# Optimization experiments

Measured on AMD Instinct MI355X. Metric: run time of the kernel, lower is better.

Reference implementation:

```python
import jax, jax.numpy as jnp
import numpy as np

N_NODES = 100000
N_EDGES = 1000000
N_GRAPHS = 5000
H = 64
F_IN = 14  # QM9 num_features (11) + pos (3)
BN_EPS = 1e-5


def setup_inputs() -> dict:
    key = jax.random.key(0)
    ks = jax.random.split(key, 16)

    def w(k, shape, fan_in):
        return (jax.random.normal(k, shape, jnp.float32) / np.sqrt(fan_in)).astype(jnp.float32)

    inp = {
        "x": jax.random.normal(ks[0], (N_NODES, 11), jnp.float32),
        "pos": jax.random.normal(ks[1], (N_NODES, 3), jnp.float32),
        "edge_index": jax.random.randint(ks[2], (2, N_EDGES), 0, N_NODES, dtype=jnp.int32),
        "batch": jnp.sort(jax.random.randint(ks[3], (N_NODES,), 0, N_GRAPHS, dtype=jnp.int32)),
    }
    dims = [F_IN, H, H]
    i = 4
    for l, din in enumerate(dims, 1):
        inp[f"w{l}a"] = w(ks[i], (din, H), din); i += 1
        inp[f"b{l}a"] = jnp.zeros((H,), jnp.float32)
        inp[f"g{l}"] = jnp.ones((H,), jnp.float32)   # BatchNorm gamma
        inp[f"be{l}"] = jnp.zeros((H,), jnp.float32)  # BatchNorm beta
        inp[f"w{l}b"] = w(ks[i], (H, H), H); i += 1
        inp[f"b{l}b"] = jnp.zeros((H,), jnp.float32)
    inp["wl1"] = w(ks[i], (3 * H, H), 3 * H); i += 1
    inp["bl1"] = jnp.zeros((H,), jnp.float32)
    inp["wl2"] = w(ks[i], (H, 1), H)
    inp["bl2"] = jnp.zeros((1,), jnp.float32)
    return inp


def _gin_layer(x, src, dst, w1, b1, g, be, w2, b2):
    # GINConv (eps=0): h = MLP(x + sum_{j in N(i)} x_j)
    agg = jax.ops.segment_sum(x[src], dst, num_segments=x.shape[0])
    h = (x + agg) @ w1 + b1
    # BatchNorm1d in training mode: batch stats over node dim (biased var)
    mu = jnp.mean(h, axis=0)
    var = jnp.mean((h - mu) ** 2, axis=0)
    h = jax.nn.relu(g * (h - mu) * jax.lax.rsqrt(var + BN_EPS) + be)
    return jax.nn.relu(h @ w2 + b2)


def _mean_pool(x, batch):
    s = jax.ops.segment_sum(x, batch, num_segments=N_GRAPHS)
    c = jax.ops.segment_sum(jnp.ones((x.shape[0], 1), x.dtype), batch, num_segments=N_GRAPHS)
    return s / jnp.maximum(c, 1.0)


def reference(x, pos, edge_index, batch,
              w1a, b1a, g1, be1, w1b, b1b,
              w2a, b2a, g2, be2, w2b, b2b,
              w3a, b3a, g3, be3, w3b, b3b,
              wl1, bl1, wl2, bl2):
    src, dst = edge_index[0], edge_index[1]
    h0 = jnp.concatenate([x, pos], axis=1)                 # [N, 14]
    x1 = _gin_layer(h0, src, dst, w1a, b1a, g1, be1, w1b, b1b)
    x2 = _gin_layer(x1, src, dst, w2a, b2a, g2, be2, w2b, b2b)
    x3 = _gin_layer(x2, src, dst, w3a, b3a, g3, be3, w3b, b3b)
    p = jnp.concatenate([_mean_pool(x1, batch), _mean_pool(x2, batch), _mean_pool(x3, batch)], axis=1)  # [G, 192]
    h = jax.nn.relu(p @ wl1 + bl1)
    return h @ wl2 + bl2                                   # [G, 1]
```

## Files before the change

### kernel.cpp

```cpp
#include <hip/hip_runtime.h>
#include <hip/hip_bf16.h>

#define BN_EPS 1e-5f
#define LDP 132
#define LDS_BF 72
#define BSH 9
#define EPB 4096

typedef short bf16x8 __attribute__((ext_vector_type(8)));
typedef float f32x4 __attribute__((ext_vector_type(4)));

__device__ __forceinline__ float loadf(const void* p, long long i, unsigned bf) {
    if (bf) return __bfloat162float(((const __hip_bfloat16*)p)[i]);
    return ((const float*)p)[i];
}
__device__ __forceinline__ float b2f(unsigned short u) {
    return __uint_as_float(((unsigned)u) << 16);
}
__device__ __forceinline__ unsigned short f2b(float f) {
    __hip_bfloat16 h = __float2bfloat16(f);
    return *(unsigned short*)&h;
}

__global__ void k_detect(const unsigned* g1w, unsigned* flag) {
    if (threadIdx.x == 0) *flag = (*g1w == 0x3F803F80u) ? 1u : 0u;
}

struct Srcs { const void* p[22]; };

__global__ void k_convert(Srcs s, const unsigned* flag, float* dst) {
    const int sizes[22] = {896,64,64,64,4096,64,  4096,64,64,64,4096,64,
                           4096,64,64,64,4096,64, 12288,64,64,1};
    const int offs[22]  = {0,896,960,1024,1088,5184, 5248,9344,9408,9472,9536,13632,
                           13696,17792,17856,17920,17984,22080, 22144,34432,34496,34560};
    int t = blockIdx.x;
    unsigned bf = *flag;
    const void* src = s.p[t];
    float* d = dst + offs[t];
    int n = sizes[t];
    for (int i = threadIdx.x; i < n; i += blockDim.x) d[i] = loadf(src, i, bf);
}

__global__ __launch_bounds__(256) void k_build(const void* x, const void* pos, const int* batch,
                        const unsigned* flag, float* h0, float* cnt, int N) {
    int i = blockIdx.x * blockDim.x + threadIdx.x;
    if (i >= N) return;
    unsigned bf = *flag;
    float v[14];
    #pragma unroll
    for (int k = 0; k < 11; k++) v[k] = loadf(x, (long long)i * 11 + k, bf);
    #pragma unroll
    for (int k = 0; k < 3; k++) v[11 + k] = loadf(pos, (long long)i * 3 + k, bf);
    #pragma unroll
    for (int k = 0; k < 14; k++) h0[(long long)i*14 + k] = v[k];
    atomicAdd(&cnt[batch[i]], 1.0f);
}

__global__ __launch_bounds__(256) void k_bhist(const int* __restrict__ ei, int* __restrict__ bcnt,
                                               int E, int NCH, int NBK) {
    __shared__ int h[1024];
    int c = blockIdx.x, t = threadIdx.x;
    for (int i = t; i < NBK; i += 256) h[i] = 0;
    __syncthreads();
    int base = c * EPB;
    for (int i = t; i < EPB; i += 256) {
        int e = base + i;
        if (e < E) atomicAdd(&h[ei[E + e] >> BSH], 1);
    }
    __syncthreads();
    for (int i = t; i < NBK; i += 256) bcnt[i * NCH + c] = h[i];
}

__global__ __launch_bounds__(256) void k_scan_partial(const int* __restrict__ src, int* partial, int M) {
    __shared__ int sr[4];
    int b = blockIdx.x, t = threadIdx.x;
    int base = b * 1024;
    int s = 0;
    #pragma unroll
    for (int k = 0; k < 4; k++) {
        int i = base + k * 256 + t;
        if (i < M) s += src[i];
    }
    #pragma unroll
    for (int off = 32; off; off >>= 1) s += __shfl_down(s, off);
    if ((t & 63) == 0) sr[t >> 6] = s;
    __syncthreads();
    if (t == 0) partial[b] = sr[0] + sr[1] + sr[2] + sr[3];
}

__global__ __launch_bounds__(1024) void k_scan_chunks(const int* partial, int* chunkoff, int nchunks) {
    __shared__ int sp[1024];
    int t = threadIdx.x;
    sp[t] = (t < nchunks) ? partial[t] : 0;
    __syncthreads();
    for (int off = 1; off < 1024; off <<= 1) {
        int v = (t >= off) ? sp[t - off] : 0;
        __syncthreads();
        sp[t] += v;
        __syncthreads();
    }
    if (t < nchunks) chunkoff[t] = (t == 0) ? 0 : sp[t - 1];
}

__global__ __launch_bounds__(256) void k_scan_final(const int* __restrict__ src, const int* chunkoff,
                                                    int* __restrict__ out, int M) {
    __shared__ int sp[256];
    int b = blockIdx.x, t = threadIdx.x;
    int base = b * 1024 + t * 4;
    int v0 = 0, v1 = 0, v2 = 0, v3 = 0;
    if (base + 0 < M) v0 = src[base + 0];
    if (base + 1 < M) v1 = src[base + 1];
    if (base + 2 < M) v2 = src[base + 2];
    if (base + 3 < M) v3 = src[base + 3];
    int s = v0 + v1 + v2 + v3;
    sp[t] = s;
    __syncthreads();
    for (int off = 1; off < 256; off <<= 1) {
        int v = (t >= off) ? sp[t - off] : 0;
        __syncthreads();
        sp[t] += v;
        __syncthreads();
    }
    int run = chunkoff[b] + sp[t] - s;
    if (base + 0 < M) { out[base + 0] = run; run += v0; }
    if (base + 1 < M) { out[base + 1] = run; run += v1; }
    if (base + 2 < M) { out[base + 2] = run; run += v2; }
    if (base + 3 < M) { out[base + 3] = run; }
}

__global__ __launch_bounds__(256) void k_place(const int* __restrict__ ei, const int* __restrict__ boff,
                                               int2* __restrict__ ebuf, int E, int NCH, int NBK) {
    __shared__ int cur[1024];
    int c = blockIdx.x, t = threadIdx.x;
    for (int i = t; i < NBK; i += 256) cur[i] = boff[i * NCH + c];
    __syncthreads();
    int base = c * EPB;
    for (int i = t; i < EPB; i += 256) {
        int e = base + i;
        if (e < E) {
            int s = ei[e], d = ei[E + e];
            int pos = atomicAdd(&cur[d >> BSH], 1);
            ebuf[pos] = make_int2(s, d);
        }
    }
}

__global__ __launch_bounds__(256) void k_bucket_fill(const int2* __restrict__ ebuf, const int* __restrict__ boff,
                                                     int* __restrict__ roff, int* __restrict__ csr,
                                                     int N, int E, int NCH, int NBK) {
    __shared__ int cnt[512];
    __shared__ int exc[512];
    __shared__ int curb[512];
    __shared__ int sp[256];
    int b = blockIdx.x, t = threadIdx.x;
    int d0 = b << BSH;
    int dpb = N - d0; if (dpb > 512) dpb = 512;
    int segS = boff[b * NCH];
    int segE = (b + 1 < NBK) ? boff[(b + 1) * NCH] : E;
    cnt[t] = 0; cnt[t + 256] = 0;
    __syncthreads();
    for (int k = segS + t; k < segE; k += 256) atomicAdd(&cnt[ebuf[k].y - d0], 1);
    __syncthreads();
    int a0 = cnt[2 * t], a1 = cnt[2 * t + 1];
    sp[t] = a0 + a1;
    __syncthreads();
    for (int off = 1; off < 256; off <<= 1) {
        int v = (t >= off) ? sp[t - off] : 0;
        __syncthreads();
        sp[t] += v;
        __syncthreads();
    }
    int pre = (t == 0) ? 0 : sp[t - 1];
    exc[2 * t] = pre; exc[2 * t + 1] = pre + a0;
    curb[2 * t] = pre; curb[2 * t + 1] = pre + a0;
    __syncthreads();
    for (int i = t; i < dpb; i += 256) roff[d0 + i] = segS + exc[i];
    if (b == NBK - 1 && t == 0) roff[N] = E;
    for (int k = segS + t; k < segE; k += 256) {
        int2 p = ebuf[k];
        int lp = atomicAdd(&curb[p.y - d0], 1);
        csr[segS + lp] = p.x;
    }
}

__global__ __launch_bounds__(256) void k_gather14(const int* __restrict__ roff, const int* __restrict__ csr,
                                                  const float* __restrict__ h0, float* __restrict__ agg, int N) {
    int g = threadIdx.x >> 4, f = threadIdx.x & 15;
    int node = blockIdx.x * 16 + g;
    if (node >= N || f >= 14) return;
    float acc = h0[(long long)node * 14 + f];
    int e0 = roff[node], e1 = roff[node + 1];
    for (int k = e0; k < e1; k++) acc += h0[(long long)csr[k] * 14 + f];
    agg[(long long)node * 14 + f] = acc;
}

__global__ __launch_bounds__(256) void k_gather64(const int* __restrict__ roff, const int* __restrict__ csr,
                                                  const unsigned short* __restrict__ xinb,
                                                  unsigned short* __restrict__ aggb, int N) {
    int g = threadIdx.x >> 4, q = threadIdx.x & 15;
    int node = blockIdx.x * 16 + g;
    if (node >= N) return;
    const ushort4* xr = (const ushort4*)xinb;
    ushort4 u = xr[(long long)node * 16 + q];
    float4 acc = make_float4(b2f(u.x), b2f(u.y), b2f(u.z), b2f(u.w));
    float4 acc2 = make_float4(0.f, 0.f, 0.f, 0.f);
    int e0 = roff[node], e1 = roff[node + 1];
    int k = e0;
    for (; k + 1 < e1; k += 2) {
        int s0 = csr[k], s1 = csr[k + 1];
        ushort4 v0 = xr[(long long)s0 * 16 + q];
        ushort4 v1 = xr[(long long)s1 * 16 + q];
        acc.x += b2f(v0.x); acc.y += b2f(v0.y); acc.z += b2f(v0.z); acc.w += b2f(v0.w);
        acc2.x += b2f(v1.x); acc2.y += b2f(v1.y); acc2.z += b2f(v1.z); acc2.w += b2f(v1.w);
    }
    if (k < e1) {
        int s0 = csr[k];
        ushort4 v0 = xr[(long long)s0 * 16 + q];
        acc.x += b2f(v0.x); acc.y += b2f(v0.y); acc.z += b2f(v0.z); acc.w += b2f(v0.w);
    }
    acc.x += acc2.x; acc.y += acc2.y; acc.z += acc2.z; acc.w += acc2.w;
    ushort4 o;
    o.x = f2b(acc.x); o.y = f2b(acc.y); o.z = f2b(acc.z); o.w = f2b(acc.w);
    *(ushort4*)&aggb[(long long)node * 64 + q * 4] = o;
}

__global__ __launch_bounds__(256) void k_mm_bn14(const float* __restrict__ S, const float* __restrict__ W,
        const float* __restrict__ bias, unsigned short* __restrict__ Hb,
        float* bnsum, float* bnsumsq, int N) {
    __shared__ float sA[14 * LDP];
    __shared__ float sW[14 * 64];
    __shared__ float sRs[4 * 64];
    __shared__ float sRq[4 * 64];
    int tid = threadIdx.x;
    int row0 = blockIdx.x * 128;
    for (int i = tid; i < 14 * 64; i += 256) sW[i] = W[i];
    int rows = N - row0; if (rows > 128) rows = 128;
    for (int i = tid; i < 128 * 14; i += 256) {
        int r = i / 14, c = i % 14;
        sA[c * LDP + r] = (r < rows) ? S[(long long)(row0 + r) * 14 + c] : 0.f;
    }
    __syncthreads();
    int tx = tid & 15, ty = tid >> 4;
    float4 bj = *(const float4*)&bias[tx * 4];
    float acc[8][4];
    #pragma unroll
    for (int i = 0; i < 8; i++) { acc[i][0] = bj.x; acc[i][1] = bj.y; acc[i][2] = bj.z; acc[i][3] = bj.w; }
    #pragma unroll
    for (int k = 0; k < 14; k++) {
        const float4 a0 = *(const float4*)&sA[k * LDP + ty * 8];
        const float4 a1 = *(const float4*)&sA[k * LDP + ty * 8 + 4];
        const float4 w  = *(const float4*)&sW[k * 64 + tx * 4];
        const float av[8] = {a0.x, a0.y, a0.z, a0.w, a1.x, a1.y, a1.z, a1.w};
        #pragma unroll
        for (int i = 0; i < 8; i++) {
            acc[i][0] += av[i] * w.x; acc[i][1] += av[i] * w.y;
            acc[i][2] += av[i] * w.z; acc[i][3] += av[i] * w.w;
        }
    }
    float cs[4] = {0.f, 0.f, 0.f, 0.f}, cq[4] = {0.f, 0.f, 0.f, 0.f};
    #pragma unroll
    for (int i = 0; i < 8; i++) {
        int r = ty * 8 + i;
        if (r < rows) {
            int gr = row0 + r;
            ushort4 hv;
            hv.x = f2b(acc[i][0]); hv.y = f2b(acc[i][1]);
            hv.z = f2b(acc[i][2]); hv.w = f2b(acc[i][3]);
            *(ushort4*)&Hb[(long long)gr * 64 + tx * 4] = hv;
            #pragma unroll
            for (int d = 0; d < 4; d++) { cs[d] += acc[i][d]; cq[d] += acc[i][d] * acc[i][d]; }
        }
    }
    #pragma unroll
    for (int d = 0; d < 4; d++) {
        cs[d] += __shfl_xor(cs[d], 16); cs[d] += __shfl_xor(cs[d], 32);
        cq[d] += __shfl_xor(cq[d], 16); cq[d] += __shfl_xor(cq[d], 32);
    }
    int wid = tid >> 6, lane = tid & 63;
    if (lane < 16) {
        #pragma unroll
        for (int d = 0; d < 4; d++) {
            sRs[wid * 64 + lane * 4 + d] = cs[d];
            sRq[wid * 64 + lane * 4 + d] = cq[d];
        }
    }
    __syncthreads();
    if (tid < 64) atomicAdd(&bnsum[tid], sRs[tid] + sRs[64 + tid] + sRs[128 + tid] + sRs[192 + tid]);
    else if (tid < 128) {
        int j = tid - 64;
        atomicAdd(&bnsumsq[j], sRq[j] + sRq[64 + j] + sRq[128 + j] + sRq[192 + j]);
    }
}

__global__ __launch_bounds__(256) void k_mm_bn64(const unsigned short* __restrict__ Sb, const float* __restrict__ W,
        const float* __restrict__ bias, unsigned short* __restrict__ Hb,
        float* bnsum, float* bnsumsq, int N) {
    __shared__ unsigned short sS[128 * LDS_BF];
    __shared__ unsigned short sWt[64 * LDS_BF];
    __shared__ float sRs[4 * 64];
    __shared__ float sRq[4 * 64];
    int tid = threadIdx.x;
    int row0 = blockIdx.x * 128;
    int rows = N - row0; if (rows > 128) rows = 128;
    #pragma unroll
    for (int it = 0; it < 8; it++) {
        int idx = tid + it * 256;
        int r = idx >> 4, q = idx & 15;
        ushort4 v = make_ushort4(0, 0, 0, 0);
        if (r < rows) v = *(const ushort4*)&Sb[(long long)(row0 + r) * 64 + (q << 2)];
        *(ushort4*)&sS[r * LDS_BF + q * 4] = v;
    }
    for (int i = tid; i < 4096; i += 256) {
        int k = i >> 6, n = i & 63;
        sWt[n * LDS_BF + k] = f2b(W[i]);
    }
    __syncthreads();
    int w = tid >> 6, lane = tid & 63;
    int half = lane >> 4, m = lane & 15;
    f32x4 acc[2][4];
    #pragma unroll
    for (int rt = 0; rt < 2; rt++)
        #pragma unroll
        for (int ct = 0; ct < 4; ct++) acc[rt][ct] = (f32x4){0.f, 0.f, 0.f, 0.f};
    #pragma unroll
    for (int km = 0; km < 2; km++) {
        bf16x8 a0 = *(const bf16x8*)&sS[(w * 32 + m) * LDS_BF + km * 32 + half * 8];
        bf16x8 a1 = *(const bf16x8*)&sS[(w * 32 + 16 + m) * LDS_BF + km * 32 + half * 8];
        #pragma unroll
        for (int ct = 0; ct < 4; ct++) {
            bf16x8 b = *(const bf16x8*)&sWt[(ct * 16 + m) * LDS_BF + km * 32 + half * 8];
            acc[0][ct] = __builtin_amdgcn_mfma_f32_16x16x32_bf16(a0, b, acc[0][ct], 0, 0, 0);
            acc[1][ct] = __builtin_amdgcn_mfma_f32_16x16x32_bf16(a1, b, acc[1][ct], 0, 0, 0);
        }
    }
    float cs[4] = {0.f, 0.f, 0.f, 0.f}, cq[4] = {0.f, 0.f, 0.f, 0.f};
    #pragma unroll
    for (int ct = 0; ct < 4; ct++) {
        float bj = bias[ct * 16 + m];
        #pragma unroll
        for (int rt = 0; rt < 2; rt++) {
            #pragma unroll
            for (int r = 0; r < 4; r++) {
                int lr = w * 32 + rt * 16 + half * 4 + r;
                if (lr < rows) {
                    float v = acc[rt][ct][r] + bj;
                    Hb[(long long)(row0 + lr) * 64 + ct * 16 + m] = f2b(v);
                    cs[ct] += v; cq[ct] += v * v;
                }
            }
        }
    }
    #pragma unroll
    for (int d = 0; d < 4; d++) {
        cs[d] += __shfl_xor(cs[d], 16); cs[d] += __shfl_xor(cs[d], 32);
        cq[d] += __shfl_xor(cq[d], 16); cq[d] += __shfl_xor(cq[d], 32);
    }
    if (lane < 16) {
        #pragma unroll
        for (int ct = 0; ct < 4; ct++) {
            sRs[w * 64 + ct * 16 + lane] = cs[ct];
            sRq[w * 64 + ct * 16 + lane] = cq[ct];
        }
    }
    __syncthreads();
    if (tid < 64) atomicAdd(&bnsum[tid], sRs[tid] + sRs[64 + tid] + sRs[128 + tid] + sRs[192 + tid]);
    else if (tid < 128) {
        int j = tid - 64;
        atomicAdd(&bnsumsq[j], sRq[j] + sRq[64 + j] + sRq[128 + j] + sRq[192 + j]);
    }
}

__global__ __launch_bounds__(256) void k_bn_mm2_rt(const unsigned short* __restrict__ Hb, const float* __restrict__ g,
        const float* __restrict__ be, const float* __restrict__ W2, const float* __restrict__ b2,
        const float* bnsum, const float* bnsumsq, const int* __restrict__ batch,
        unsigned short* __restrict__ xout, float* pool, int N, float invN, int loff) {
    __shared__ unsigned short sS[128 * LDS_BF];
    __shared__ unsigned short sWt[64 * LDS_BF];
    __shared__ float sSc[64];
    __shared__ float sSh[64];
    int tid = threadIdx.x;
    int row0 = blockIdx.x * 128;
    int rows = N - row0; if (rows > 128) rows = 128;
    if (tid < 64) {
        float mu = bnsum[tid] * invN;
        float var = bnsumsq[tid] * invN - mu * mu;
        float sc = g[tid] * rsqrtf(var + BN_EPS);
        sSc[tid] = sc; sSh[tid] = be[tid] - sc * mu;
    }
    for (int i = tid; i < 4096; i += 256) {
        int k = i >> 6, n = i & 63;
        sWt[n * LDS_BF + k] = f2b(W2[i]);
    }
    __syncthreads();
    #pragma unroll
    for (int it = 0; it < 8; it++) {
        int idx = tid + it * 256;
        int r = idx >> 4, q = idx & 15;
        ushort4 o = make_ushort4(0, 0, 0, 0);
        if (r < rows) {
            ushort4 u = *(const ushort4*)&Hb[(long long)(row0 + r) * 64 + (q << 2)];
            o.x = f2b(fmaxf(sSc[q*4+0] * b2f(u.x) + sSh[q*4+0], 0.f));
            o.y = f2b(fmaxf(sSc[q*4+1] * b2f(u.y) + sSh[q*4+1], 0.f));
            o.z = f2b(fmaxf(sSc[q*4+2] * b2f(u.z) + sSh[q*4+2], 0.f));
            o.w = f2b(fmaxf(sSc[q*4+3] * b2f(u.w) + sSh[q*4+3], 0.f));
        }
        *(ushort4*)&sS[r * LDS_BF + q * 4] = o;
    }
    __syncthreads();
    int w = tid >> 6, lane = tid & 63;
    int half = lane >> 4, m = lane & 15;
    f32x4 acc[2][4];
    #pragma unroll
    for (int rt = 0; rt < 2; rt++)
        #pragma unroll
        for (int ct = 0; ct < 4; ct++) acc[rt][ct] = (f32x4){0.f, 0.f, 0.f, 0.f};
    #pragma unroll
    for (int km = 0; km < 2; km++) {
        bf16x8 a0 = *(const bf16x8*)&sS[(w * 32 + m) * LDS_BF + km * 32 + half * 8];
        bf16x8 a1 = *(const bf16x8*)&sS[(w * 32 + 16 + m) * LDS_BF + km * 32 + half * 8];
        #pragma unroll
        for (int ct = 0; ct < 4; ct++) {
            bf16x8 b = *(const bf16x8*)&sWt[(ct * 16 + m) * LDS_BF + km * 32 + half * 8];
            acc[0][ct] = __builtin_amdgcn_mfma_f32_16x16x32_bf16(a0, b, acc[0][ct], 0, 0, 0);
            acc[1][ct] = __builtin_amdgcn_mfma_f32_16x16x32_bf16(a1, b, acc[1][ct], 0, 0, 0);
        }
    }
    float b2j[4];
    #pragma unroll
    for (int ct = 0; ct < 4; ct++) b2j[ct] = b2[ct * 16 + m];
    int prevg = -1;
    float p[4] = {0.f, 0.f, 0.f, 0.f};
    #pragma unroll
    for (int rt = 0; rt < 2; rt++) {
        #pragma unroll
        for (int r = 0; r < 4; r++) {
            int lr = w * 32 + rt * 16 + half * 4 + r;
            if (lr < rows) {
                int gr = row0 + lr;
                float o[4];
                #pragma unroll
                for (int ct = 0; ct < 4; ct++) {
                    o[ct] = fmaxf(acc[rt][ct][r] + b2j[ct], 0.f);
                    if (xout) xout[(long long)gr * 64 + ct * 16 + m] = f2b(o[ct]);
                }
                int gid = batch[gr];
                if (gid != prevg) {
                    if (prevg >= 0) {
                        float* pp = &pool[(long long)prevg * 192 + loff + m];
                        atomicAdd(pp + 0,  p[0]); atomicAdd(pp + 16, p[1]);
                        atomicAdd(pp + 32, p[2]); atomicAdd(pp + 48, p[3]);
                    }
                    prevg = gid;
                    p[0] = o[0]; p[1] = o[1]; p[2] = o[2]; p[3] = o[3];
                } else {
                    p[0] += o[0]; p[1] += o[1]; p[2] += o[2]; p[3] += o[3];
                }
            }
        }
    }
    if (prevg >= 0) {
        float* pp = &pool[(long long)prevg * 192 + loff + m];
        atomicAdd(pp + 0,  p[0]); atomicAdd(pp + 16, p[1]);
        atomicAdd(pp + 32, p[2]); atomicAdd(pp + 48, p[3]);
    }
}

__global__ __launch_bounds__(64) void k_head(const float* pool, const float* cnt,
                        const float* wl1, const float* bl1, const float* wl2, const float* bl2,
                        const unsigned* flag, void* out, int G) {
    int gb = blockIdx.x; int j = threadIdx.x;
    if (gb >= G) return;
    __shared__ float sP[192];
    float c = fmaxf(cnt[gb], 1.0f);
    float inv = 1.0f / c;
    for (int k = j; k < 192; k += 64) sP[k] = pool[(long long)gb * 192 + k] * inv;
    __syncthreads();
    float acc = bl1[j];
    for (int k = 0; k < 192; k++) acc += sP[k] * wl1[k * 64 + j];
    float v = fmaxf(acc, 0.f) * wl2[j];
    #pragma unroll
    for (int off = 32; off; off >>= 1) v += __shfl_down(v, off);
    if (j == 0) {
        float res = v + bl2[0];
        if (*flag) ((__hip_bfloat16*)out)[gb] = __float2bfloat16(res);
        else       ((float*)out)[gb] = res;
    }
}

extern "C" void kernel_launch(void* const* d_in, const int* in_sizes, int n_in,
                              void* d_out, int out_size, void* d_ws, size_t ws_size,
                              hipStream_t stream) {
    const void* x   = d_in[0];
    const void* pos = d_in[1];
    const int* ei    = (const int*)d_in[2];
    const int* batch = (const int*)d_in[3];
    const int N = in_sizes[3];
    const int E = in_sizes[2] / 2;
    const int G = out_size;

    float* ws = (float*)d_ws;
    unsigned* flag = (unsigned*)ws;
    float* P = ws + 16;
    float* w1a = P + 0;     float* b1a = P + 896;   float* g1 = P + 960;   float* be1 = P + 1024;
    float* w1b = P + 1088;  float* b1b = P + 5184;
    float* w2a = P + 5248;  float* b2a = P + 9344;  float* g2 = P + 9408;  float* be2 = P + 9472;
    float* w2b = P + 9536;  float* b2b = P + 13632;
    float* w3a = P + 13696; float* b3a = P + 17792; float* g3 = P + 17856; float* be3 = P + 17920;
    float* w3b = P + 17984; float* b3b = P + 22080;
    float* wl1 = P + 22144; float* bl1 = P + 34432; float* wl2 = P + 34496; float* bl2 = P + 34560;

    long long off = 16 + 34592;
    float* h0   = ws + off;                 off += (long long)N * 14;
    float* agg  = ws + off;                 off += (long long)N * 64;
    float* Hbuf = ws + off;                 off += (long long)N * 64;
    float* curf = ws + off;                 off += (long long)N * 64;
    float* pool = ws + off;                 off += (long long)G * 192;
    float* cnt  = ws + off;                 off += G;
    float* bn   = ws + off;                 off += 128;
    int*   roff = (int*)(ws + off);
    int* csr = roff + (N + 1);

    unsigned short* curh = (unsigned short*)curf;
    unsigned short* aggh = (unsigned short*)agg;
    unsigned short* Hh   = (unsigned short*)Hbuf;

    const int NBK = (N + 511) >> BSH;
    const int NCH = (E + EPB - 1) / EPB;
    const int M = NBK * NCH;
    int* bcnt     = csr + E;
    int* boff     = bcnt + M;
    int* partial  = boff + M;
    int* chunkoff = partial + 1024;
    int2* ebuf = (int2*)Hbuf;

    hipMemsetAsync(pool, 0, ((size_t)G * 192 + (size_t)G) * sizeof(float), stream);

    k_detect<<<1, 1, 0, stream>>>((const unsigned*)d_in[6], flag);

    Srcs s;
    for (int i = 0; i < 22; i++) s.p[i] = d_in[4 + i];
    k_convert<<<22, 256, 0, stream>>>(s, flag, P);

    int nb = (N + 255) / 256;
    k_build<<<nb, 256, 0, stream>>>(x, pos, batch, flag, h0, cnt, N);

    k_bhist<<<NCH, 256, 0, stream>>>(ei, bcnt, E, NCH, NBK);
    int nchS = (M + 1023) / 1024;
    k_scan_partial<<<nchS, 256, 0, stream>>>(bcnt, partial, M);
    k_scan_chunks<<<1, 1024, 0, stream>>>(partial, chunkoff, nchS);
    k_scan_final<<<nchS, 256, 0, stream>>>(bcnt, chunkoff, boff, M);
    k_place<<<NCH, 256, 0, stream>>>(ei, boff, ebuf, E, NCH, NBK);
    k_bucket_fill<<<NBK, 256, 0, stream>>>(ebuf, boff, roff, csr, N, E, NCH, NBK);

    int rtBlocks = (N + 127) / 128;
    int gBlocks = (N + 15) / 16;
    float invN = 1.0f / (float)N;

    k_gather14<<<gBlocks, 256, 0, stream>>>(roff, csr, h0, agg, N);
    hipMemsetAsync(bn, 0, 128 * sizeof(float), stream);
    k_mm_bn14<<<rtBlocks, 256, 0, stream>>>(agg, w1a, b1a, Hh, bn, bn + 64, N);
    k_bn_mm2_rt<<<rtBlocks, 256, 0, stream>>>(Hh, g1, be1, w1b, b1b, bn, bn + 64, batch,
                                              curh, pool, N, invN, 0);
    k_gather64<<<gBlocks, 256, 0, stream>>>(roff, csr, curh, aggh, N);
    hipMemsetAsync(bn, 0, 128 * sizeof(float), stream);
    k_mm_bn64<<<rtBlocks, 256, 0, stream>>>(aggh, w2a, b2a, Hh, bn, bn + 64, N);
    k_bn_mm2_rt<<<rtBlocks, 256, 0, stream>>>(Hh, g2, be2, w2b, b2b, bn, bn + 64, batch,
                                              curh, pool, N, invN, 64);
    k_gather64<<<gBlocks, 256, 0, stream>>>(roff, csr, curh, aggh, N);
    hipMemsetAsync(bn, 0, 128 * sizeof(float), stream);
    k_mm_bn64<<<rtBlocks, 256, 0, stream>>>(aggh, w3a, b3a, Hh, bn, bn + 64, N);
    k_bn_mm2_rt<<<rtBlocks, 256, 0, stream>>>(Hh, g3, be3, w3b, b3b, bn, bn + 64, batch,
                                              nullptr, pool, N, invN, 128);

    k_head<<<G, 64, 0, stream>>>(pool, cnt, wl1, bl1, wl2, bl2, flag, d_out, G);
}
```

Baseline: 387.2 us.

## Fuse CSR neighbor gather into first-matmul BN kernels and store h0 as bf16

Removes the separate gather kernels and performs the neighbor sum aggregation directly inside the first-matmul+BN-stat kernels, writing the aggregated rows straight into shared memory. This avoids writing and re-reading the N x 64 (and N x 14) aggregate buffers and drops kernel launches. The layer-1 input is also stored as padded bf16 (16 shorts per row) so the gather reads half the bytes. The trade-off is lower parallelism per gather (one 128-row block now handles all row gathers with fewer threads per row) and an added bf16 rounding of the raw input features.

New measurement: 393.1 us. About the same (+1.5%).

```diff
diff --git a/kernel.cpp b/kernel.cpp
--- a/kernel.cpp
+++ b/kernel.cpp
@@ -21,6 +21,8 @@
     __hip_bfloat16 h = __float2bfloat16(f);
     return *(unsigned short*)&h;
 }
+__device__ __forceinline__ float blo(unsigned u) { return __uint_as_float(u << 16); }
+__device__ __forceinline__ float bhi(unsigned u) { return __uint_as_float(u & 0xffff0000u); }
 
 __global__ void k_detect(const unsigned* g1w, unsigned* flag) {
     if (threadIdx.x == 0) *flag = (*g1w == 0x3F803F80u) ? 1u : 0u;
@@ -42,17 +44,19 @@
 }
 
 __global__ __launch_bounds__(256) void k_build(const void* x, const void* pos, const int* batch,
-                        const unsigned* flag, float* h0, float* cnt, int N) {
+                        const unsigned* flag, unsigned short* h0b, float* cnt, int N) {
     int i = blockIdx.x * blockDim.x + threadIdx.x;
     if (i >= N) return;
     unsigned bf = *flag;
-    float v[14];
-    #pragma unroll
-    for (int k = 0; k < 11; k++) v[k] = loadf(x, (long long)i * 11 + k, bf);
-    #pragma unroll
-    for (int k = 0; k < 3; k++) v[11 + k] = loadf(pos, (long long)i * 3 + k, bf);
-    #pragma unroll
-    for (int k = 0; k < 14; k++) h0[(long long)i*14 + k] = v[k];
+    unsigned short v[16];
+    #pragma unroll
+    for (int k = 0; k < 11; k++) v[k] = f2b(loadf(x, (long long)i * 11 + k, bf));
+    #pragma unroll
+    for (int k = 0; k < 3; k++) v[11 + k] = f2b(loadf(pos, (long long)i * 3 + k, bf));
+    v[14] = 0; v[15] = 0;
+    #pragma unroll
+    for (int k = 0; k < 4; k++)
+        *(ushort4*)&h0b[(long long)i * 16 + k * 4] = make_ushort4(v[4*k], v[4*k+1], v[4*k+2], v[4*k+3]);
     atomicAdd(&cnt[batch[i]], 1.0f);
 }
 
@@ -183,48 +187,8 @@
     }
 }
 
-__global__ __launch_bounds__(256) void k_gather14(const int* __restrict__ roff, const int* __restrict__ csr,
-                                                  const float* __restrict__ h0, float* __restrict__ agg, int N) {
-    int g = threadIdx.x >> 4, f = threadIdx.x & 15;
-    int node = blockIdx.x * 16 + g;
-    if (node >= N || f >= 14) return;
-    float acc = h0[(long long)node * 14 + f];
-    int e0 = roff[node], e1 = roff[node + 1];
-    for (int k = e0; k < e1; k++) acc += h0[(long long)csr[k] * 14 + f];
-    agg[(long long)node * 14 + f] = acc;
-}
-
-__global__ __launch_bounds__(256) void k_gather64(const int* __restrict__ roff, const int* __restrict__ csr,
-                                                  const unsigned short* __restrict__ xinb,
-                                                  unsigned short* __restrict__ aggb, int N) {
-    int g = threadIdx.x >> 4, q = threadIdx.x & 15;
-    int node = blockIdx.x * 16 + g;
-    if (node >= N) return;
-    const ushort4* xr = (const ushort4*)xinb;
-    ushort4 u = xr[(long long)node * 16 + q];
-    float4 acc = make_float4(b2f(u.x), b2f(u.y), b2f(u.z), b2f(u.w));
-    float4 acc2 = make_float4(0.f, 0.f, 0.f, 0.f);
-    int e0 = roff[node], e1 = roff[node + 1];
-    int k = e0;
-    for (; k + 1 < e1; k += 2) {
-        int s0 = csr[k], s1 = csr[k + 1];
-        ushort4 v0 = xr[(long long)s0 * 16 + q];
-        ushort4 v1 = xr[(long long)s1 * 16 + q];
-        acc.x += b2f(v0.x); acc.y += b2f(v0.y); acc.z += b2f(v0.z); acc.w += b2f(v0.w);
-        acc2.x += b2f(v1.x); acc2.y += b2f(v1.y); acc2.z += b2f(v1.z); acc2.w += b2f(v1.w);
-    }
-    if (k < e1) {
-        int s0 = csr[k];
-        ushort4 v0 = xr[(long long)s0 * 16 + q];
-        acc.x += b2f(v0.x); acc.y += b2f(v0.y); acc.z += b2f(v0.z); acc.w += b2f(v0.w);
-    }
-    acc.x += acc2.x; acc.y += acc2.y; acc.z += acc2.z; acc.w += acc2.w;
-    ushort4 o;
-    o.x = f2b(acc.x); o.y = f2b(acc.y); o.z = f2b(acc.z); o.w = f2b(acc.w);
-    *(ushort4*)&aggb[(long long)node * 64 + q * 4] = o;
-}
-
-__global__ __launch_bounds__(256) void k_mm_bn14(const float* __restrict__ S, const float* __restrict__ W,
+__global__ __launch_bounds__(256) void k_gmm_bn14(const int* __restrict__ roff, const int* __restrict__ csr,
+        const unsigned short* __restrict__ h0b, const float* __restrict__ W,
         const float* __restrict__ bias, unsigned short* __restrict__ Hb,
         float* bnsum, float* bnsumsq, int N) {
     __shared__ float sA[14 * LDP];
@@ -233,11 +197,35 @@
     __shared__ float sRq[4 * 64];
     int tid = threadIdx.x;
     int row0 = blockIdx.x * 128;
+    int rows = N - row0; if (rows > 128) rows = 128;
     for (int i = tid; i < 14 * 64; i += 256) sW[i] = W[i];
-    int rows = N - row0; if (rows > 128) rows = 128;
-    for (int i = tid; i < 128 * 14; i += 256) {
-        int r = i / 14, c = i % 14;
-        sA[c * LDP + r] = (r < rows) ? S[(long long)(row0 + r) * 14 + c] : 0.f;
+    const unsigned* h0u = (const unsigned*)h0b;
+    int q = tid & 7, nn = tid >> 3;
+    #pragma unroll
+    for (int it = 0; it < 4; it++) {
+        int r = nn + it * 32;
+        float a0 = 0.f, a1 = 0.f;
+        if (r < rows) {
+            int gr = row0 + r;
+            unsigned su = h0u[(long long)gr * 8 + q];
+            a0 = blo(su); a1 = bhi(su);
+            int e0 = roff[gr], e1 = roff[gr + 1];
+            int k = e0;
+            float b0 = 0.f, b1 = 0.f;
+            for (; k + 1 < e1; k += 2) {
+                unsigned u0 = h0u[(long long)csr[k] * 8 + q];
+                unsigned u1 = h0u[(long long)csr[k + 1] * 8 + q];
+                a0 += blo(u0); a1 += bhi(u0);
+                b0 += blo(u1); b1 += bhi(u1);
+            }
+            if (k < e1) {
+                unsigned u0 = h0u[(long long)csr[k] * 8 + q];
+                a0 += blo(u0); a1 += bhi(u0);
+            }
+            a0 += b0; a1 += b1;
+        }
+        if (2 * q < 14)     sA[(2 * q) * LDP + r] = a0;
+        if (2 * q + 1 < 14) sA[(2 * q + 1) * LDP + r] = a1;
     }
     __syncthreads();
     int tx = tid & 15, ty = tid >> 4;
@@ -292,7 +280,8 @@
     }
 }
 
-__global__ __launch_bounds__(256) void k_mm_bn64(const unsigned short* __restrict__ Sb, const float* __restrict__ W,
+__global__ __launch_bounds__(256) void k_gmm_bn64(const int* __restrict__ roff, const int* __restrict__ csr,
+        const unsigned short* __restrict__ xinb, const float* __restrict__ W,
         const float* __restrict__ bias, unsigned short* __restrict__ Hb,
         float* bnsum, float* bnsumsq, int N) {
     __shared__ unsigned short sS[128 * LDS_BF];
@@ -302,17 +291,40 @@
     int tid = threadIdx.x;
     int row0 = blockIdx.x * 128;
     int rows = N - row0; if (rows > 128) rows = 128;
-    #pragma unroll
-    for (int it = 0; it < 8; it++) {
-        int idx = tid + it * 256;
-        int r = idx >> 4, q = idx & 15;
-        ushort4 v = make_ushort4(0, 0, 0, 0);
-        if (r < rows) v = *(const ushort4*)&Sb[(long long)(row0 + r) * 64 + (q << 2)];
-        *(ushort4*)&sS[r * LDS_BF + q * 4] = v;
-    }
     for (int i = tid; i < 4096; i += 256) {
         int k = i >> 6, n = i & 63;
         sWt[n * LDS_BF + k] = f2b(W[i]);
+    }
+    const ushort4* xr = (const ushort4*)xinb;
+    int q = tid & 15, nn = tid >> 4;
+    #pragma unroll
+    for (int it = 0; it < 8; it++) {
+        int r = nn + it * 16;
+        float4 acc = make_float4(0.f, 0.f, 0.f, 0.f);
+        if (r < rows) {
+            int gr = row0 + r;
+            ushort4 u = xr[(long long)gr * 16 + q];
+            acc = make_float4(b2f(u.x), b2f(u.y), b2f(u.z), b2f(u.w));
+            float4 acc2 = make_float4(0.f, 0.f, 0.f, 0.f);
+            int e0 = roff[gr], e1 = roff[gr + 1];
+            int k = e0;
+            for (; k + 1 < e1; k += 2) {
+                int s0 = csr[k], s1 = csr[k + 1];
+                ushort4 v0 = xr[(long long)s0 * 16 + q];
+                ushort4 v1 = xr[(long long)s1 * 16 + q];
+                acc.x += b2f(v0.x); acc.y += b2f(v0.y); acc.z += b2f(v0.z); acc.w += b2f(v0.w);
+                acc2.x += b2f(v1.x); acc2.y += b2f(v1.y); acc2.z += b2f(v1.z); acc2.w += b2f(v1.w);
+            }
+            if (k < e1) {
+                int s0 = csr[k];
+                ushort4 v0 = xr[(long long)s0 * 16 + q];
+                acc.x += b2f(v0.x); acc.y += b2f(v0.y); acc.z += b2f(v0.z); acc.w += b2f(v0.w);
+            }
+            acc.x += acc2.x; acc.y += acc2.y; acc.z += acc2.z; acc.w += acc2.w;
+        }
+        ushort4 o;
+        o.x = f2b(acc.x); o.y = f2b(acc.y); o.z = f2b(acc.z); o.w = f2b(acc.w);
+        *(ushort4*)&sS[r * LDS_BF + q * 4] = o;
     }
     __syncthreads();
     int w = tid >> 6, lane = tid & 63;
@@ -510,8 +522,8 @@
     float* wl1 = P + 22144; float* bl1 = P + 34432; float* wl2 = P + 34496; float* bl2 = P + 34560;
 
     long long off = 16 + 34592;
-    float* h0   = ws + off;                 off += (long long)N * 14;
-    float* agg  = ws + off;                 off += (long long)N * 64;
+    float* h0r  = ws + off;                 off += (long long)N * 14;
+    float* aggr = ws + off;                 off += (long long)N * 64;
     float* Hbuf = ws + off;                 off += (long long)N * 64;
     float* curf = ws + off;                 off += (long long)N * 64;
     float* pool = ws + off;                 off += (long long)G * 192;
@@ -520,8 +532,8 @@
     int*   roff = (int*)(ws + off);
     int* csr = roff + (N + 1);
 
+    unsigned short* h0b  = (unsigned short*)h0r;
     unsigned short* curh = (unsigned short*)curf;
-    unsigned short* aggh = (unsigned short*)agg;
     unsigned short* Hh   = (unsigned short*)Hbuf;
 
     const int NBK = (N + 511) >> BSH;
@@ -542,7 +554,7 @@
     k_convert<<<22, 256, 0, stream>>>(s, flag, P);
 
     int nb = (N + 255) / 256;
-    k_build<<<nb, 256, 0, stream>>>(x, pos, batch, flag, h0, cnt, N);
+    k_build<<<nb, 256, 0, stream>>>(x, pos, batch, flag, h0b, cnt, N);
 
     k_bhist<<<NCH, 256, 0, stream>>>(ei, bcnt, E, NCH, NBK);
     int nchS = (M + 1023) / 1024;
@@ -553,22 +565,18 @@
     k_bucket_fill<<<NBK, 256, 0, stream>>>(ebuf, boff, roff, csr, N, E, NCH, NBK);
 
     int rtBlocks = (N + 127) / 128;
-    int gBlocks = (N + 15) / 16;
     float invN = 1.0f / (float)N;
 
-    k_gather14<<<gBlocks, 256, 0, stream>>>(roff, csr, h0, agg, N);
     hipMemsetAsync(bn, 0, 128 * sizeof(float), stream);
-    k_mm_bn14<<<rtBlocks, 256, 0, stream>>>(agg, w1a, b1a, Hh, bn, bn + 64, N);
+    k_gmm_bn14<<<rtBlocks, 256, 0, stream>>>(roff, csr, h0b, w1a, b1a, Hh, bn, bn + 64, N);
     k_bn_mm2_rt<<<rtBlocks, 256, 0, stream>>>(Hh, g1, be1, w1b, b1b, bn, bn + 64, batch,
                                               curh, pool, N, invN, 0);
-    k_gather64<<<gBlocks, 256, 0, stream>>>(roff, csr, curh, aggh, N);
     hipMemsetAsync(bn, 0, 128 * sizeof(float), stream);
-    k_mm_bn64<<<rtBlocks, 256, 0, stream>>>(aggh, w2a, b2a, Hh, bn, bn + 64, N);
+    k_gmm_bn64<<<rtBlocks, 256, 0, stream>>>(roff, csr, curh, w2a, b2a, Hh, bn, bn + 64, N);
     k_bn_mm2_rt<<<rtBlocks, 256, 0, stream>>>(Hh, g2, be2, w2b, b2b, bn, bn + 64, batch,
                                               curh, pool, N, invN, 64);
-    k_gather64<<<gBlocks, 256, 0, stream>>>(roff, csr, curh, aggh, N);
     hipMemsetAsync(bn, 0, 128 * sizeof(float), stream);
-    k_mm_bn64<<<rtBlocks, 256, 0, stream>>>(aggh, w3a, b3a, Hh, bn, bn + 64, N);
+    k_gmm_bn64<<<rtBlocks, 256, 0, stream>>>(roff, csr, curh, w3a, b3a, Hh, bn, bn + 64, N);
     k_bn_mm2_rt<<<rtBlocks, 256, 0, stream>>>(Hh, g3, be3, w3b, b3b, bn, bn + 64, batch,
                                               nullptr, pool, N, invN, 128);
 
```
